# Optimization experiments

Measured on AMD Instinct MI355X. Metric: run time of the kernel, lower is better.

The kernel has to match this reference:

```python
import jax, jax.numpy as jnp
import numpy as np

DIM = 512
HEADS = 8
DIM_HEAD = 64
INNER = HEADS * DIM_HEAD  # 512
EPS = 1e-5


def setup_inputs() -> dict:
    key = jax.random.key(0)
    ks = jax.random.split(key, 8)
    b, n = 4, 2048
    x = jax.random.normal(ks[0], (b, n, DIM), dtype=jnp.float32)
    ln_g = jnp.ones((DIM,), jnp.float32)
    ln_b = jnp.zeros((DIM,), jnp.float32)
    w_qkv = jax.random.normal(ks[1], (DIM, 3 * INNER), jnp.float32) * (DIM ** -0.5)
    reattn_w = jax.random.normal(ks[2], (HEADS, HEADS), jnp.float32)
    rn_g = jnp.ones((HEADS,), jnp.float32)
    rn_b = jnp.zeros((HEADS,), jnp.float32)
    w_out = jax.random.normal(ks[3], (INNER, DIM), jnp.float32) * (INNER ** -0.5)
    b_out = jnp.zeros((DIM,), jnp.float32)
    return {"x": x, "ln_g": ln_g, "ln_b": ln_b, "w_qkv": w_qkv,
            "reattn_w": reattn_w, "rn_g": rn_g, "rn_b": rn_b,
            "w_out": w_out, "b_out": b_out}


def _layernorm(x, g, b, axis=-1):
    mu = jnp.mean(x, axis=axis, keepdims=True)
    var = jnp.var(x, axis=axis, keepdims=True)
    return (x - mu) * jax.lax.rsqrt(var + EPS) * g + b


def reference(x, ln_g, ln_b, w_qkv, reattn_w, rn_g, rn_b, w_out, b_out):
    b, n, _ = x.shape
    h, d = HEADS, DIM_HEAD
    scale = d ** -0.5
    xn = _layernorm(x, ln_g, ln_b)                       # [b,n,dim]
    qkv = xn @ w_qkv                                     # [b,n,3*inner]
    q, k, v = jnp.split(qkv, 3, axis=-1)
    to_heads = lambda t: t.reshape(b, n, h, d).transpose(0, 2, 1, 3)  # [b,h,n,d]
    q, k, v = to_heads(q), to_heads(k), to_heads(v)
    dots = jnp.einsum('bhid,bhjd->bhij', q, k) * scale   # [b,h,n,n]
    attn = jax.nn.softmax(dots, axis=-1)
    # cross-head re-attention mixing
    attn = jnp.einsum('bhij,hg->bgij', attn, reattn_w)
    # LayerNorm over the head axis (axis=1), affine params shaped [h]
    attn = _layernorm(attn, rn_g[None, :, None, None], rn_b[None, :, None, None], axis=1)
    out = jnp.einsum('bhij,bhjd->bhid', attn, v)         # [b,h,n,d]
    out = out.transpose(0, 2, 1, 3).reshape(b, n, h * d)
    return out @ w_out + b_out
```

## Files before the change

kernel.cpp:

```cpp
#include <hip/hip_runtime.h>
#include <hip/hip_bf16.h>
#include <math.h>

#define DEV __device__ __forceinline__

typedef short bf16x8 __attribute__((ext_vector_type(8)));
typedef short bf16x4 __attribute__((ext_vector_type(4)));
typedef float f32x4 __attribute__((ext_vector_type(4)));

static const int Nn = 2048;
static const int DIMd = 512;

DEV float bf2f(short u) {
    union { unsigned int i; float f; } c;
    c.i = ((unsigned int)(unsigned short)u) << 16;
    return c.f;
}

DEV short f2bf(float f) {
    union { float f; unsigned int i; } c;
    c.f = f;
    unsigned int u = c.i;
    unsigned int r = (u + 0x7fffu + ((u >> 16) & 1u)) >> 16;
    return (short)r;
}

DEV void gload16(const short* __restrict__ g, short* l) {
    __builtin_amdgcn_global_load_lds(
        (__attribute__((address_space(1))) void*)g,
        (__attribute__((address_space(3))) void*)l, 16, 0, 0);
}

__global__ void k_transpose_cast(const float* __restrict__ src,
                                 short* __restrict__ dst, int K, int N) {
    int o = blockIdx.x * 256 + threadIdx.x;
    if (o >= K * N) return;
    int n = o / K, k = o - n * K;
    dst[o] = f2bf(src[(size_t)k * N + n]);
}

__global__ __launch_bounds__(256) void k_ln(const float* __restrict__ x,
                                            const float* __restrict__ g,
                                            const float* __restrict__ bta,
                                            short* __restrict__ xn) {
    int row = blockIdx.x * 4 + (threadIdx.x >> 6);
    int lane = threadIdx.x & 63;
    const float* xr = x + (size_t)row * DIMd;
    float4 v0 = ((const float4*)xr)[lane * 2];
    float4 v1 = ((const float4*)xr)[lane * 2 + 1];
    float f[8] = {v0.x, v0.y, v0.z, v0.w, v1.x, v1.y, v1.z, v1.w};
    float s = 0.f, sq = 0.f;
#pragma unroll
    for (int t = 0; t < 8; ++t) { s += f[t]; sq += f[t] * f[t]; }
#pragma unroll
    for (int off = 32; off >= 1; off >>= 1) {
        s += __shfl_xor(s, off);
        sq += __shfl_xor(sq, off);
    }
    float mu = s * (1.0f / 512.0f);
    float var = sq * (1.0f / 512.0f) - mu * mu;
    float rs = rsqrtf(var + 1e-5f);
    bf16x8 o;
#pragma unroll
    for (int t = 0; t < 8; ++t) {
        int c = lane * 8 + t;
        o[t] = f2bf((f[t] - mu) * rs * g[c] + bta[c]);
    }
    *(bf16x8*)(xn + (size_t)row * DIMd + lane * 8) = o;
}

DEV void gemm128_loop(const short* __restrict__ A, const short* __restrict__ B,
                      int K, int i0, int n0, int tid,
                      short* As, short* Bs, f32x4 acc[4][4]) {
    const int w = tid >> 6, wr = w >> 1, wc = w & 1;
    const int lane = tid & 63, fr = lane & 15, fq = lane >> 4;
    const int sr = tid >> 3, sc = (tid & 7) * 8;
    for (int k0 = 0; k0 < K; k0 += 64) {
#pragma unroll
        for (int L = 0; L < 4; ++L) {
            gload16(A + (size_t)(i0 + L * 32 + sr) * K + k0 + sc,
                    As + (L * 32 + sr) * 64 + sc);
            gload16(B + (size_t)(n0 + L * 32 + sr) * K + k0 + sc,
                    Bs + (L * 32 + sr) * 64 + sc);
        }
        __syncthreads();
#pragma unroll
        for (int kk = 0; kk < 2; ++kk) {
            bf16x8 af[4], bfr[4];
#pragma unroll
            for (int m = 0; m < 4; ++m)
                af[m] = *(const bf16x8*)(As + (wr * 64 + m * 16 + fr) * 64 + kk * 32 + fq * 8);
#pragma unroll
            for (int n = 0; n < 4; ++n)
                bfr[n] = *(const bf16x8*)(Bs + (wc * 64 + n * 16 + fr) * 64 + kk * 32 + fq * 8);
#pragma unroll
            for (int m = 0; m < 4; ++m)
#pragma unroll
                for (int n = 0; n < 4; ++n)
                    acc[m][n] = __builtin_amdgcn_mfma_f32_16x16x32_bf16(af[m], bfr[n], acc[m][n], 0, 0, 0);
        }
        __syncthreads();
    }
}

__global__ __launch_bounds__(256) void k_qkv(const short* __restrict__ xn,
                                             const short* __restrict__ wT,
                                             short* __restrict__ Q,
                                             short* __restrict__ Kb,
                                             short* __restrict__ Vt) {
    __shared__ short As[128 * 64], Bs[128 * 64];
    int tid = threadIdx.x;
    int i0 = blockIdx.x * 128, n0 = blockIdx.y * 128;
    f32x4 acc[4][4] = {};
    gemm128_loop(xn, wT, DIMd, i0, n0, tid, As, Bs, acc);
    const int w = tid >> 6, wr = w >> 1, wc = w & 1;
    const int lane = tid & 63, fr = lane & 15, fq = lane >> 4;
#pragma unroll
    for (int m = 0; m < 4; ++m) {
#pragma unroll
        for (int n = 0; n < 4; ++n) {
#pragma unroll
            for (int r = 0; r < 4; ++r) {
                int row = i0 + wr * 64 + m * 16 + fq * 4 + r;
                int c = n0 + wc * 64 + n * 16 + fr;
                short hv = f2bf(acc[m][n][r]);
                int b = row >> 11, i = row & 2047;
                int t = c >> 9, rem = c & 511;
                int h = rem >> 6, dd = rem & 63;
                size_t bh = (size_t)(b * 8 + h);
                if (t == 0)      Q [(bh * Nn + i) * 64 + dd] = hv;
                else if (t == 1) Kb[(bh * Nn + i) * 64 + dd] = hv;
                else             Vt[(bh * 64 + dd) * Nn + i] = hv;
            }
        }
    }
}

__global__ __launch_bounds__(256) void k_out(const short* __restrict__ outh,
                                             const short* __restrict__ wT,
                                             const float* __restrict__ bias,
                                             float* __restrict__ out) {
    __shared__ short As[128 * 64], Bs[128 * 64];
    int tid = threadIdx.x;
    int i0 = blockIdx.x * 128, n0 = blockIdx.y * 128;
    f32x4 acc[4][4] = {};
    gemm128_loop(outh, wT, 512, i0, n0, tid, As, Bs, acc);
    const int w = tid >> 6, wr = w >> 1, wc = w & 1;
    const int lane = tid & 63, fr = lane & 15, fq = lane >> 4;
#pragma unroll
    for (int m = 0; m < 4; ++m)
#pragma unroll
        for (int n = 0; n < 4; ++n)
#pragma unroll
            for (int r = 0; r < 4; ++r) {
                int row = i0 + wr * 64 + m * 16 + fq * 4 + r;
                int c = n0 + wc * 64 + n * 16 + fr;
                out[(size_t)row * 512 + c] = acc[m][n][r] + bias[c];
            }
}

DEV void decode_bid2(int bid, int& b, int& i0, int& jh) {
    int xcd = bid & 7, slot = bid >> 3;
    b = xcd >> 1;
    jh = xcd & 1;
    i0 = slot * 32;
}

__global__ __launch_bounds__(512)
__attribute__((amdgpu_waves_per_eu(4, 4)))
void k_stats(const short* __restrict__ Q,
             const short* __restrict__ Kb,
             float* __restrict__ mpart,
             float* __restrict__ lpart) {
    int b, i0, jh;
    decode_bid2(blockIdx.x, b, i0, jh);
    int tid = threadIdx.x, wv = tid >> 6, lane = tid & 63;
    int fr = lane & 15, fq = lane >> 4;
    size_t bh = (size_t)(b * 8 + wv);
    const short* qb = Q + (bh * Nn + i0) * 64;
    bf16x8 qf[2][2];
#pragma unroll
    for (int in = 0; in < 2; ++in)
#pragma unroll
        for (int kk = 0; kk < 2; ++kk)
            qf[in][kk] = *(const bf16x8*)(qb + (in * 16 + fr) * 64 + kk * 32 + fq * 8);
    float m[2] = {-1e30f, -1e30f}, l[2] = {0.f, 0.f};
    const short* kbase = Kb + bh * Nn * 64 + (size_t)jh * 1024 * 64;
    for (int jt = 0; jt < 16; ++jt) {
        const short* kb = kbase + jt * 64 * 64;
        f32x4 acc[4][2] = {};
#pragma unroll
        for (int kk = 0; kk < 2; ++kk)
#pragma unroll
            for (int jm = 0; jm < 4; ++jm) {
                bf16x8 kf = *(const bf16x8*)(kb + (jm * 16 + fr) * 64 + kk * 32 + fq * 8);
                acc[jm][0] = __builtin_amdgcn_mfma_f32_16x16x32_bf16(kf, qf[0][kk], acc[jm][0], 0, 0, 0);
                acc[jm][1] = __builtin_amdgcn_mfma_f32_16x16x32_bf16(kf, qf[1][kk], acc[jm][1], 0, 0, 0);
            }
#pragma unroll
        for (int in = 0; in < 2; ++in) {
            float mt = acc[0][in][0];
#pragma unroll
            for (int jm = 0; jm < 4; ++jm)
#pragma unroll
                for (int r = 0; r < 4; ++r) mt = fmaxf(mt, acc[jm][in][r]);
            mt = fmaxf(mt, __shfl_xor(mt, 16));
            mt = fmaxf(mt, __shfl_xor(mt, 32));
            float es = 0.f;
#pragma unroll
            for (int jm = 0; jm < 4; ++jm)
#pragma unroll
                for (int r = 0; r < 4; ++r)
                    es += __expf((acc[jm][in][r] - mt) * 0.125f);
            es += __shfl_xor(es, 16);
            es += __shfl_xor(es, 32);
            float mn = fmaxf(m[in], mt);
            l[in] = l[in] * __expf((m[in] - mn) * 0.125f) + es * __expf((mt - mn) * 0.125f);
            m[in] = mn;
        }
    }
    if (fq == 0) {
#pragma unroll
        for (int in = 0; in < 2; ++in) {
            size_t o = (size_t)jh * 65536 + bh * Nn + i0 + in * 16 + fr;
            mpart[o] = m[in];
            lpart[o] = l[in];
        }
    }
}

__global__ __launch_bounds__(256) void k_zcomb(const float* __restrict__ mpart,
                                               const float* __restrict__ lpart,
                                               float* __restrict__ zstat) {
    int idx = blockIdx.x * 256 + threadIdx.x;
    float m0 = mpart[idx], m1 = mpart[65536 + idx];
    float l0 = lpart[idx], l1 = lpart[65536 + idx];
    float M = fmaxf(m0, m1);
    float L = l0 * __expf((m0 - M) * 0.125f) + l1 * __expf((m1 - M) * 0.125f);
    zstat[idx] = M * 0.125f + __logf(L);
}

__global__ __launch_bounds__(512)
__attribute__((amdgpu_waves_per_eu(4, 4)))
void k_fused(const short* __restrict__ Q, const short* __restrict__ Kb,
             const short* __restrict__ Vt, const float* __restrict__ zstat,
             const float* __restrict__ R, const float* __restrict__ rg,
             const float* __restrict__ rb, float* __restrict__ opart) {
    __shared__ short S_lds[8 * 32 * 64];
    __shared__ short P_lds[8 * 32 * 64];
    __shared__ float Rraw[64], Rc[64], rgs[8], rbs[8], zl[8 * 32];
    int b, i0, jh;
    decode_bid2(blockIdx.x, b, i0, jh);
    int tid = threadIdx.x, wv = tid >> 6, lane = tid & 63;
    int fr = lane & 15, fq = lane >> 4;
    if (tid < 64) Rraw[tid] = R[tid];
    if (tid < 8) { rgs[tid] = rg[tid]; rbs[tid] = rb[tid]; }
    if (tid >= 64 && tid < 320) {
        int q = tid - 64;
        zl[q] = zstat[(size_t)(b * 8 + (q >> 5)) * Nn + i0 + (q & 31)];
    }
    __syncthreads();
    if (tid < 64) {
        int h = tid >> 3;
        float mn = 0.f;
#pragma unroll
        for (int gg = 0; gg < 8; ++gg) mn += Rraw[h * 8 + gg];
        Rc[tid] = Rraw[tid] - mn * 0.125f;
    }
    size_t bh = (size_t)(b * 8 + wv);
    const short* qb = Q + (bh * Nn + i0) * 64;
    bf16x8 qf[2][2];
#pragma unroll
    for (int in = 0; in < 2; ++in)
#pragma unroll
        for (int kk = 0; kk < 2; ++kk)
            qf[in][kk] = *(const bf16x8*)(qb + (in * 16 + fr) * 64 + kk * 32 + fq * 8);
    float zh[2] = {zl[wv * 32 + fr], zl[wv * 32 + 16 + fr]};
    const short* kbase = Kb + bh * Nn * 64 + (size_t)jh * 1024 * 64;
    const short* vbase = Vt + bh * 64 * Nn + (size_t)jh * 1024;
    const int mi = tid >> 4, j4 = (tid & 15) * 4;
    const int msw = (mi & 7) << 4;
    f32x4 acc_o[2][4] = {};
    for (int jt = 0; jt < 16; ++jt) {
        {
            const short* kb = kbase + jt * 64 * 64;
            f32x4 acc[4][2] = {};
#pragma unroll
            for (int kk = 0; kk < 2; ++kk)
#pragma unroll
                for (int jm = 0; jm < 4; ++jm) {
                    bf16x8 kf = *(const bf16x8*)(kb + (jm * 16 + fr) * 64 + kk * 32 + fq * 8);
                    acc[jm][0] = __builtin_amdgcn_mfma_f32_16x16x32_bf16(kf, qf[0][kk], acc[jm][0], 0, 0, 0);
                    acc[jm][1] = __builtin_amdgcn_mfma_f32_16x16x32_bf16(kf, qf[1][kk], acc[jm][1], 0, 0, 0);
                }
#pragma unroll
            for (int in = 0; in < 2; ++in) {
                int i = in * 16 + fr;
                int sw = (i & 7) << 4;
#pragma unroll
                for (int jm = 0; jm < 4; ++jm) {
                    bf16x4 pk;
#pragma unroll
                    for (int r = 0; r < 4; ++r)
                        pk[r] = f2bf(__expf(acc[jm][in][r] * 0.125f - zh[in]));
                    int j0 = jm * 16 + fq * 4;
                    *(bf16x4*)((char*)S_lds + wv * 4096 + i * 128 + ((j0 * 2) ^ sw)) = pk;
                }
            }
        }
        __syncthreads();
        {
            bf16x4 sh[8];
#pragma unroll
            for (int h = 0; h < 8; ++h)
                sh[h] = *(const bf16x4*)((char*)S_lds + h * 4096 + mi * 128 + ((j4 * 2) ^ msw));
            bf16x4 og[8];
#pragma unroll
            for (int e = 0; e < 4; ++e) {
                float pv[8];
#pragma unroll
                for (int h = 0; h < 8; ++h) pv[h] = bf2f(sh[h][e]);
                float cc[8];
#pragma unroll
                for (int gg = 0; gg < 8; ++gg) {
                    float s = 0.f;
#pragma unroll
                    for (int h = 0; h < 8; ++h) s += pv[h] * Rc[h * 8 + gg];
                    cc[gg] = s;
                }
                float var = 0.f;
#pragma unroll
                for (int gg = 0; gg < 8; ++gg) var += cc[gg] * cc[gg];
                var *= 0.125f;
                float rs_ = rsqrtf(var + 1e-5f);
#pragma unroll
                for (int gg = 0; gg < 8; ++gg)
                    og[gg][e] = f2bf(cc[gg] * rs_ * rgs[gg] + rbs[gg]);
            }
#pragma unroll
            for (int gg = 0; gg < 8; ++gg)
                *(bf16x4*)((char*)P_lds + gg * 4096 + mi * 128 + ((j4 * 2) ^ msw)) = og[gg];
        }
        __syncthreads();
        {
            const short* vb = vbase + jt * 64;
#pragma unroll
            for (int kk = 0; kk < 2; ++kk) {
                bf16x8 vf[4];
#pragma unroll
                for (int dn = 0; dn < 4; ++dn)
                    vf[dn] = *(const bf16x8*)(vb + (size_t)(dn * 16 + fr) * Nn + kk * 32 + fq * 8);
#pragma unroll
                for (int im = 0; im < 2; ++im) {
                    int row = im * 16 + fr;
                    bf16x8 pa = *(const bf16x8*)((char*)P_lds + wv * 4096 + row * 128 +
                                                 (((kk * 32 + fq * 8) * 2) ^ ((row & 7) << 4)));
#pragma unroll
                    for (int dn = 0; dn < 4; ++dn)
                        acc_o[im][dn] = __builtin_amdgcn_mfma_f32_16x16x32_bf16(pa, vf[dn], acc_o[im][dn], 0, 0, 0);
                }
            }
        }
        __syncthreads();
    }
    float* po = opart + (size_t)jh * 4194304 + ((size_t)b * Nn + i0) * 512;
#pragma unroll
    for (int im = 0; im < 2; ++im)
#pragma unroll
        for (int dn = 0; dn < 4; ++dn)
#pragma unroll
            for (int r = 0; r < 4; ++r)
                po[(im * 16 + fq * 4 + r) * 512 + wv * 64 + dn * 16 + fr] = acc_o[im][dn][r];
}

__global__ __launch_bounds__(256) void k_osum(const float* __restrict__ opart,
                                              short* __restrict__ outh) {
    int base = (blockIdx.x * 256 + threadIdx.x) * 4;
    f32x4 a = *(const f32x4*)(opart + base);
    f32x4 c = *(const f32x4*)(opart + 4194304 + base);
    bf16x4 o;
#pragma unroll
    for (int t = 0; t < 4; ++t) o[t] = f2bf(a[t] + c[t]);
    *(bf16x4*)(outh + base) = o;
}

extern "C" void kernel_launch(void* const* d_in, const int* in_sizes, int n_in,
                              void* d_out, int out_size, void* d_ws, size_t ws_size,
                              hipStream_t stream) {
    const float* x      = (const float*)d_in[0];
    const float* ln_g   = (const float*)d_in[1];
    const float* ln_b   = (const float*)d_in[2];
    const float* w_qkv  = (const float*)d_in[3];
    const float* reattn = (const float*)d_in[4];
    const float* rn_g   = (const float*)d_in[5];
    const float* rn_b   = (const float*)d_in[6];
    const float* w_out  = (const float*)d_in[7];
    const float* b_out  = (const float*)d_in[8];
    float* out = (float*)d_out;

    char* ws = (char*)d_ws;
    short* wqkvT = (short*)ws; ws += (size_t)1536 * 512 * 2;
    short* woutT = (short*)ws; ws += (size_t)512 * 512 * 2;
    short* xn    = (short*)ws; ws += (size_t)8192 * 512 * 2;
    short* Q     = (short*)ws; ws += (size_t)32 * 2048 * 64 * 2;
    short* Kb    = (short*)ws; ws += (size_t)32 * 2048 * 64 * 2;
    short* Vt    = (short*)ws; ws += (size_t)32 * 64 * 2048 * 2;
    short* outh  = (short*)ws; ws += (size_t)8192 * 512 * 2;
    float* opart = (float*)ws; ws += (size_t)2 * 4194304 * 4;
    float* mpart = (float*)ws; ws += (size_t)2 * 65536 * 4;
    float* lpart = (float*)ws; ws += (size_t)2 * 65536 * 4;
    float* zstat = (float*)xn;

    k_transpose_cast<<<(512 * 1536 + 255) / 256, 256, 0, stream>>>(w_qkv, wqkvT, 512, 1536);
    k_transpose_cast<<<(512 * 512 + 255) / 256, 256, 0, stream>>>(w_out, woutT, 512, 512);
    k_ln<<<8192 / 4, 256, 0, stream>>>(x, ln_g, ln_b, xn);
    k_qkv<<<dim3(8192 / 128, 1536 / 128), 256, 0, stream>>>(xn, wqkvT, Q, Kb, Vt);

    k_stats<<<512, 512, 0, stream>>>(Q, Kb, mpart, lpart);
    k_zcomb<<<256, 256, 0, stream>>>(mpart, lpart, zstat);
    k_fused<<<512, 512, 0, stream>>>(Q, Kb, Vt, zstat, reattn, rn_g, rn_b, opart);
    k_osum<<<4096, 256, 0, stream>>>(opart, outh);

    k_out<<<dim3(8192 / 128, 512 / 128), 256, 0, stream>>>(outh, woutT, b_out, out);
}
```

Measured before the change: 341.8 us.

## Double-buffer S/P LDS tiles and overlap next QK^T with head mixing

Splits the S and P shared-memory tiles into two buffers so the QK^T and exp of the next key tile runs in the same phase as the cross-head mix and layernorm of the current tile. This removes one of the three block barriers per iteration and prefetches K fragments into registers early. The cost is twice the LDS footprint (about 128KB) and more live registers, which forces the waves-per-EU hint down from 4 to 2 and so lowers occupancy.

```diff
diff --git a/kernel.cpp b/kernel.cpp
--- a/kernel.cpp
+++ b/kernel.cpp
@@ -241,13 +241,13 @@
 }
 
 __global__ __launch_bounds__(512)
-__attribute__((amdgpu_waves_per_eu(4, 4)))
+__attribute__((amdgpu_waves_per_eu(2, 2)))
 void k_fused(const short* __restrict__ Q, const short* __restrict__ Kb,
              const short* __restrict__ Vt, const float* __restrict__ zstat,
              const float* __restrict__ R, const float* __restrict__ rg,
              const float* __restrict__ rb, float* __restrict__ opart) {
-    __shared__ short S_lds[8 * 32 * 64];
-    __shared__ short P_lds[8 * 32 * 64];
+    __shared__ short S_lds[2][8 * 32 * 64];
+    __shared__ short P_lds[2][8 * 32 * 64];
     __shared__ float Rraw[64], Rc[64], rgs[8], rbs[8], zl[8 * 32];
     int b, i0, jh;
     decode_bid2(blockIdx.x, b, i0, jh);
@@ -281,39 +281,54 @@
     const int mi = tid >> 4, j4 = (tid & 15) * 4;
     const int msw = (mi & 7) << 4;
     f32x4 acc_o[2][4] = {};
-    for (int jt = 0; jt < 16; ++jt) {
-        {
-            const short* kb = kbase + jt * 64 * 64;
-            f32x4 acc[4][2] = {};
+
+    {
+        const short* kb = kbase;
+        f32x4 acc[4][2] = {};
+#pragma unroll
+        for (int kk = 0; kk < 2; ++kk)
+#pragma unroll
+            for (int jm = 0; jm < 4; ++jm) {
+                bf16x8 kf = *(const bf16x8*)(kb + (jm * 16 + fr) * 64 + kk * 32 + fq * 8);
+                acc[jm][0] = __builtin_amdgcn_mfma_f32_16x16x32_bf16(kf, qf[0][kk], acc[jm][0], 0, 0, 0);
+                acc[jm][1] = __builtin_amdgcn_mfma_f32_16x16x32_bf16(kf, qf[1][kk], acc[jm][1], 0, 0, 0);
+            }
+        char* Sw = (char*)S_lds[0];
+#pragma unroll
+        for (int in = 0; in < 2; ++in) {
+            int i = in * 16 + fr;
+            int sw = (i & 7) << 4;
+#pragma unroll
+            for (int jm = 0; jm < 4; ++jm) {
+                bf16x4 pk;
+#pragma unroll
+                for (int r = 0; r < 4; ++r)
+                    pk[r] = f2bf(__expf(acc[jm][in][r] * 0.125f - zh[in]));
+                int j0 = jm * 16 + fq * 4;
+                *(bf16x4*)(Sw + wv * 4096 + i * 128 + ((j0 * 2) ^ sw)) = pk;
+            }
+        }
+    }
+    __syncthreads();
+
+    for (int k = 0; k < 16; ++k) {
+        const int cur = k & 1;
+        char* Scur = (char*)S_lds[cur];
+        char* Pcur = (char*)P_lds[cur];
+        bf16x8 kreg[2][4];
+        if (k < 15) {
+            const short* kb = kbase + (k + 1) * 64 * 64;
 #pragma unroll
             for (int kk = 0; kk < 2; ++kk)
 #pragma unroll
-                for (int jm = 0; jm < 4; ++jm) {
-                    bf16x8 kf = *(const bf16x8*)(kb + (jm * 16 + fr) * 64 + kk * 32 + fq * 8);
-                    acc[jm][0] = __builtin_amdgcn_mfma_f32_16x16x32_bf16(kf, qf[0][kk], acc[jm][0], 0, 0, 0);
-                    acc[jm][1] = __builtin_amdgcn_mfma_f32_16x16x32_bf16(kf, qf[1][kk], acc[jm][1], 0, 0, 0);
-                }
-#pragma unroll
-            for (int in = 0; in < 2; ++in) {
-                int i = in * 16 + fr;
-                int sw = (i & 7) << 4;
-#pragma unroll
-                for (int jm = 0; jm < 4; ++jm) {
-                    bf16x4 pk;
-#pragma unroll
-                    for (int r = 0; r < 4; ++r)
-                        pk[r] = f2bf(__expf(acc[jm][in][r] * 0.125f - zh[in]));
-                    int j0 = jm * 16 + fq * 4;
-                    *(bf16x4*)((char*)S_lds + wv * 4096 + i * 128 + ((j0 * 2) ^ sw)) = pk;
-                }
-            }
-        }
-        __syncthreads();
+                for (int jm = 0; jm < 4; ++jm)
+                    kreg[kk][jm] = *(const bf16x8*)(kb + (jm * 16 + fr) * 64 + kk * 32 + fq * 8);
+        }
         {
             bf16x4 sh[8];
 #pragma unroll
             for (int h = 0; h < 8; ++h)
-                sh[h] = *(const bf16x4*)((char*)S_lds + h * 4096 + mi * 128 + ((j4 * 2) ^ msw));
+                sh[h] = *(const bf16x4*)(Scur + h * 4096 + mi * 128 + ((j4 * 2) ^ msw));
             bf16x4 og[8];
 #pragma unroll
             for (int e = 0; e < 4; ++e) {
@@ -339,11 +354,36 @@
             }
 #pragma unroll
             for (int gg = 0; gg < 8; ++gg)
-                *(bf16x4*)((char*)P_lds + gg * 4096 + mi * 128 + ((j4 * 2) ^ msw)) = og[gg];
+                *(bf16x4*)(Pcur + gg * 4096 + mi * 128 + ((j4 * 2) ^ msw)) = og[gg];
+        }
+        if (k < 15) {
+            char* Snxt = (char*)S_lds[cur ^ 1];
+            f32x4 acc[4][2] = {};
+#pragma unroll
+            for (int kk = 0; kk < 2; ++kk)
+#pragma unroll
+                for (int jm = 0; jm < 4; ++jm) {
+                    acc[jm][0] = __builtin_amdgcn_mfma_f32_16x16x32_bf16(kreg[kk][jm], qf[0][kk], acc[jm][0], 0, 0, 0);
+                    acc[jm][1] = __builtin_amdgcn_mfma_f32_16x16x32_bf16(kreg[kk][jm], qf[1][kk], acc[jm][1], 0, 0, 0);
+                }
+#pragma unroll
+            for (int in = 0; in < 2; ++in) {
+                int i = in * 16 + fr;
+                int sw = (i & 7) << 4;
+#pragma unroll
+                for (int jm = 0; jm < 4; ++jm) {
+                    bf16x4 pk;
+#pragma unroll
+                    for (int r = 0; r < 4; ++r)
+                        pk[r] = f2bf(__expf(acc[jm][in][r] * 0.125f - zh[in]));
+                    int j0 = jm * 16 + fq * 4;
+                    *(bf16x4*)(Snxt + wv * 4096 + i * 128 + ((j0 * 2) ^ sw)) = pk;
+                }
+            }
         }
         __syncthreads();
         {
-            const short* vb = vbase + jt * 64;
+            const short* vb = vbase + k * 64;
 #pragma unroll
             for (int kk = 0; kk < 2; ++kk) {
                 bf16x8 vf[4];
@@ -353,7 +393,7 @@
 #pragma unroll
                 for (int im = 0; im < 2; ++im) {
                     int row = im * 16 + fr;
-                    bf16x8 pa = *(const bf16x8*)((char*)P_lds + wv * 4096 + row * 128 +
+                    bf16x8 pa = *(const bf16x8*)(Pcur + wv * 4096 + row * 128 +
                                                  (((kk * 32 + fq * 8) * 2) ^ ((row & 7) << 4)));
 #pragma unroll
                     for (int dn = 0; dn < 4; ++dn)
@@ -361,7 +401,6 @@
                 }
             }
         }
-        __syncthreads();
     }
     float* po = opart + (size_t)jh * 4194304 + ((size_t)b * Nn + i0) * 512;
 #pragma unroll
```

New measurement: 479.4 us. 1.4x slower.

## Double-buffer S/P tiles in fused attention and fold softmax scale into Q

Applied to the files above, without the earlier changes.

Folds the 1/sqrt(d) softmax scale into Q when the QKV GEMM writes its output, which removes the per-element multiplies from both the stats pass and the fused pass. The fused kernel now double-buffers the S and P LDS tiles and software-pipelines the loop, so the PV MFMA for tile k runs in the same phase as the QK/exp work for tile k+1. This drops one barrier per iteration. In exchange, LDS use doubles, and occupancy is lowered from 4 to 2 waves per EU, which may reduce latency hiding.

```diff
diff --git a/kernel.cpp b/kernel.cpp
--- a/kernel.cpp
+++ b/kernel.cpp
@@ -123,14 +123,14 @@
             for (int r = 0; r < 4; ++r) {
                 int row = i0 + wr * 64 + m * 16 + fq * 4 + r;
                 int c = n0 + wc * 64 + n * 16 + fr;
-                short hv = f2bf(acc[m][n][r]);
+                float v = acc[m][n][r];
                 int b = row >> 11, i = row & 2047;
                 int t = c >> 9, rem = c & 511;
                 int h = rem >> 6, dd = rem & 63;
                 size_t bh = (size_t)(b * 8 + h);
-                if (t == 0)      Q [(bh * Nn + i) * 64 + dd] = hv;
-                else if (t == 1) Kb[(bh * Nn + i) * 64 + dd] = hv;
-                else             Vt[(bh * 64 + dd) * Nn + i] = hv;
+                if (t == 0)      Q [(bh * Nn + i) * 64 + dd] = f2bf(v * 0.125f);
+                else if (t == 1) Kb[(bh * Nn + i) * 64 + dd] = f2bf(v);
+                else             Vt[(bh * 64 + dd) * Nn + i] = f2bf(v);
             }
         }
     }
@@ -211,11 +211,11 @@
             for (int jm = 0; jm < 4; ++jm)
 #pragma unroll
                 for (int r = 0; r < 4; ++r)
-                    es += __expf((acc[jm][in][r] - mt) * 0.125f);
+                    es += __expf(acc[jm][in][r] - mt);
             es += __shfl_xor(es, 16);
             es += __shfl_xor(es, 32);
             float mn = fmaxf(m[in], mt);
-            l[in] = l[in] * __expf((m[in] - mn) * 0.125f) + es * __expf((mt - mn) * 0.125f);
+            l[in] = l[in] * __expf(m[in] - mn) + es * __expf(mt - mn);
             m[in] = mn;
         }
     }
@@ -236,18 +236,18 @@
     float m0 = mpart[idx], m1 = mpart[65536 + idx];
     float l0 = lpart[idx], l1 = lpart[65536 + idx];
     float M = fmaxf(m0, m1);
-    float L = l0 * __expf((m0 - M) * 0.125f) + l1 * __expf((m1 - M) * 0.125f);
-    zstat[idx] = M * 0.125f + __logf(L);
+    float L = l0 * __expf(m0 - M) + l1 * __expf(m1 - M);
+    zstat[idx] = M + __logf(L);
 }
 
 __global__ __launch_bounds__(512)
-__attribute__((amdgpu_waves_per_eu(4, 4)))
+__attribute__((amdgpu_waves_per_eu(2, 2)))
 void k_fused(const short* __restrict__ Q, const short* __restrict__ Kb,
              const short* __restrict__ Vt, const float* __restrict__ zstat,
              const float* __restrict__ R, const float* __restrict__ rg,
              const float* __restrict__ rb, float* __restrict__ opart) {
-    __shared__ short S_lds[8 * 32 * 64];
-    __shared__ short P_lds[8 * 32 * 64];
+    __shared__ short S_lds[2][8 * 32 * 64];
+    __shared__ short P_lds[2][8 * 32 * 64];
     __shared__ float Rraw[64], Rc[64], rgs[8], rbs[8], zl[8 * 32];
     int b, i0, jh;
     decode_bid2(blockIdx.x, b, i0, jh);
@@ -281,88 +281,96 @@
     const int mi = tid >> 4, j4 = (tid & 15) * 4;
     const int msw = (mi & 7) << 4;
     f32x4 acc_o[2][4] = {};
-    for (int jt = 0; jt < 16; ++jt) {
-        {
-            const short* kb = kbase + jt * 64 * 64;
-            f32x4 acc[4][2] = {};
-#pragma unroll
-            for (int kk = 0; kk < 2; ++kk)
-#pragma unroll
-                for (int jm = 0; jm < 4; ++jm) {
-                    bf16x8 kf = *(const bf16x8*)(kb + (jm * 16 + fr) * 64 + kk * 32 + fq * 8);
-                    acc[jm][0] = __builtin_amdgcn_mfma_f32_16x16x32_bf16(kf, qf[0][kk], acc[jm][0], 0, 0, 0);
-                    acc[jm][1] = __builtin_amdgcn_mfma_f32_16x16x32_bf16(kf, qf[1][kk], acc[jm][1], 0, 0, 0);
-                }
-#pragma unroll
-            for (int in = 0; in < 2; ++in) {
-                int i = in * 16 + fr;
-                int sw = (i & 7) << 4;
-#pragma unroll
-                for (int jm = 0; jm < 4; ++jm) {
-                    bf16x4 pk;
-#pragma unroll
-                    for (int r = 0; r < 4; ++r)
-                        pk[r] = f2bf(__expf(acc[jm][in][r] * 0.125f - zh[in]));
-                    int j0 = jm * 16 + fq * 4;
-                    *(bf16x4*)((char*)S_lds + wv * 4096 + i * 128 + ((j0 * 2) ^ sw)) = pk;
-                }
-            }
-        }
+
+    auto phaseA = [&](int jt, char* Sdst) {
+        const short* kb = kbase + jt * 64 * 64;
+        f32x4 acc[4][2] = {};
+#pragma unroll
+        for (int kk = 0; kk < 2; ++kk)
+#pragma unroll
+            for (int jm = 0; jm < 4; ++jm) {
+                bf16x8 kf = *(const bf16x8*)(kb + (jm * 16 + fr) * 64 + kk * 32 + fq * 8);
+                acc[jm][0] = __builtin_amdgcn_mfma_f32_16x16x32_bf16(kf, qf[0][kk], acc[jm][0], 0, 0, 0);
+                acc[jm][1] = __builtin_amdgcn_mfma_f32_16x16x32_bf16(kf, qf[1][kk], acc[jm][1], 0, 0, 0);
+            }
+#pragma unroll
+        for (int in = 0; in < 2; ++in) {
+            int i = in * 16 + fr;
+            int sw = (i & 7) << 4;
+#pragma unroll
+            for (int jm = 0; jm < 4; ++jm) {
+                bf16x4 pk;
+#pragma unroll
+                for (int r = 0; r < 4; ++r)
+                    pk[r] = f2bf(__expf(acc[jm][in][r] - zh[in]));
+                int j0 = jm * 16 + fq * 4;
+                *(bf16x4*)(Sdst + wv * 4096 + i * 128 + ((j0 * 2) ^ sw)) = pk;
+            }
+        }
+    };
+    auto phaseB = [&](char* Ssrc, char* Pdst) {
+        bf16x4 sh[8];
+#pragma unroll
+        for (int h = 0; h < 8; ++h)
+            sh[h] = *(const bf16x4*)(Ssrc + h * 4096 + mi * 128 + ((j4 * 2) ^ msw));
+        bf16x4 og[8];
+#pragma unroll
+        for (int e = 0; e < 4; ++e) {
+            float pv[8];
+#pragma unroll
+            for (int h = 0; h < 8; ++h) pv[h] = bf2f(sh[h][e]);
+            float cc[8];
+#pragma unroll
+            for (int gg = 0; gg < 8; ++gg) {
+                float s = 0.f;
+#pragma unroll
+                for (int h = 0; h < 8; ++h) s += pv[h] * Rc[h * 8 + gg];
+                cc[gg] = s;
+            }
+            float var = 0.f;
+#pragma unroll
+            for (int gg = 0; gg < 8; ++gg) var += cc[gg] * cc[gg];
+            var *= 0.125f;
+            float rs_ = rsqrtf(var + 1e-5f);
+#pragma unroll
+            for (int gg = 0; gg < 8; ++gg)
+                og[gg][e] = f2bf(cc[gg] * rs_ * rgs[gg] + rbs[gg]);
+        }
+#pragma unroll
+        for (int gg = 0; gg < 8; ++gg)
+            *(bf16x4*)(Pdst + gg * 4096 + mi * 128 + ((j4 * 2) ^ msw)) = og[gg];
+    };
+    auto phaseC = [&](int jt, char* Psrc) {
+        const short* vb = vbase + jt * 64;
+#pragma unroll
+        for (int kk = 0; kk < 2; ++kk) {
+            bf16x8 vf[4];
+#pragma unroll
+            for (int dn = 0; dn < 4; ++dn)
+                vf[dn] = *(const bf16x8*)(vb + (size_t)(dn * 16 + fr) * Nn + kk * 32 + fq * 8);
+#pragma unroll
+            for (int im = 0; im < 2; ++im) {
+                int row = im * 16 + fr;
+                bf16x8 pa = *(const bf16x8*)(Psrc + wv * 4096 + row * 128 +
+                                             (((kk * 32 + fq * 8) * 2) ^ ((row & 7) << 4)));
+#pragma unroll
+                for (int dn = 0; dn < 4; ++dn)
+                    acc_o[im][dn] = __builtin_amdgcn_mfma_f32_16x16x32_bf16(pa, vf[dn], acc_o[im][dn], 0, 0, 0);
+            }
+        }
+    };
+
+    phaseA(0, (char*)S_lds[0]);
+    __syncthreads();
+    phaseB((char*)S_lds[0], (char*)P_lds[0]);
+    for (int k = 0; k < 16; ++k) {
         __syncthreads();
-        {
-            bf16x4 sh[8];
-#pragma unroll
-            for (int h = 0; h < 8; ++h)
-                sh[h] = *(const bf16x4*)((char*)S_lds + h * 4096 + mi * 128 + ((j4 * 2) ^ msw));
-            bf16x4 og[8];
-#pragma unroll
-            for (int e = 0; e < 4; ++e) {
-                float pv[8];
-#pragma unroll
-                for (int h = 0; h < 8; ++h) pv[h] = bf2f(sh[h][e]);
-                float cc[8];
-#pragma unroll
-                for (int gg = 0; gg < 8; ++gg) {
-                    float s = 0.f;
-#pragma unroll
-                    for (int h = 0; h < 8; ++h) s += pv[h] * Rc[h * 8 + gg];
-                    cc[gg] = s;
-                }
-                float var = 0.f;
-#pragma unroll
-                for (int gg = 0; gg < 8; ++gg) var += cc[gg] * cc[gg];
-                var *= 0.125f;
-                float rs_ = rsqrtf(var + 1e-5f);
-#pragma unroll
-                for (int gg = 0; gg < 8; ++gg)
-                    og[gg][e] = f2bf(cc[gg] * rs_ * rgs[gg] + rbs[gg]);
-            }
-#pragma unroll
-            for (int gg = 0; gg < 8; ++gg)
-                *(bf16x4*)((char*)P_lds + gg * 4096 + mi * 128 + ((j4 * 2) ^ msw)) = og[gg];
-        }
+        phaseC(k, (char*)P_lds[k & 1]);
+        if (k < 15) phaseA(k + 1, (char*)S_lds[(k + 1) & 1]);
         __syncthreads();
-        {
-            const short* vb = vbase + jt * 64;
-#pragma unroll
-            for (int kk = 0; kk < 2; ++kk) {
-                bf16x8 vf[4];
-#pragma unroll
-                for (int dn = 0; dn < 4; ++dn)
-                    vf[dn] = *(const bf16x8*)(vb + (size_t)(dn * 16 + fr) * Nn + kk * 32 + fq * 8);
-#pragma unroll
-                for (int im = 0; im < 2; ++im) {
-                    int row = im * 16 + fr;
-                    bf16x8 pa = *(const bf16x8*)((char*)P_lds + wv * 4096 + row * 128 +
-                                                 (((kk * 32 + fq * 8) * 2) ^ ((row & 7) << 4)));
-#pragma unroll
-                    for (int dn = 0; dn < 4; ++dn)
-                        acc_o[im][dn] = __builtin_amdgcn_mfma_f32_16x16x32_bf16(pa, vf[dn], acc_o[im][dn], 0, 0, 0);
-                }
-            }
-        }
-        __syncthreads();
-    }
+        if (k < 15) phaseB((char*)S_lds[(k + 1) & 1], (char*)P_lds[(k + 1) & 1]);
+    }
+
     float* po = opart + (size_t)jh * 4194304 + ((size_t)b * Nn + i0) * 512;
 #pragma unroll
     for (int im = 0; im < 2; ++im)
```

Measured after the change: 329.2 us. 1.04x faster.
